# Performance work log

Measured on AMD Instinct MI355X. Metric: run time of the kernel, lower is better.

## Reference

```python
import jax, jax.numpy as jnp
import numpy as np
from jax import lax

B, T, D, H, HODE = 1024, 128, 64, 256, 256
DT = 0.1  # times spaced by 0.1 == integration_step_size -> one RK4 step per interval


def setup_inputs() -> dict:
    key = jax.random.key(0)
    ks = jax.random.split(key, 10)
    s = lambda fan: 1.0 / np.sqrt(fan)
    return {
        "x": jax.random.normal(ks[0], (B, T, D), jnp.float32),
        "times": jnp.arange(T, dtype=jnp.float32) * DT,
        "mask": (jax.random.uniform(ks[1], (B, T)) > 0.3).astype(jnp.float32),
        # ODE MLP: Linear(H->HODE), ReLU, Linear(HODE->H)
        "W1": jax.random.uniform(ks[2], (HODE, H), jnp.float32, -s(H), s(H)),
        "b1": jax.random.uniform(ks[3], (HODE,), jnp.float32, -s(H), s(H)),
        "W2": jax.random.uniform(ks[4], (H, HODE), jnp.float32, -s(HODE), s(HODE)),
        "b2": jax.random.uniform(ks[5], (H,), jnp.float32, -s(HODE), s(HODE)),
        # GRUCell params (torch layout: [3H, D]/[3H, H], gate order r,z,n)
        "W_ih": jax.random.uniform(ks[6], (3 * H, D), jnp.float32, -s(H), s(H)),
        "b_ih": jax.random.uniform(ks[7], (3 * H,), jnp.float32, -s(H), s(H)),
        "W_hh": jax.random.uniform(ks[8], (3 * H, H), jnp.float32, -s(H), s(H)),
        "b_hh": jax.random.uniform(ks[9], (3 * H,), jnp.float32, -s(H), s(H)),
    }


def _ode_gru_forward(x, times, mask, W1, b1, W2, b2, W_ih, b_ih, W_hh, b_hh):
    Bs, Ts, _ = x.shape
    Hs = W_hh.shape[1]

    def f(h):  # autonomous ODE vector field: MLP(h)
        return jnp.maximum(h @ W1.T + b1, 0.0) @ W2.T + b2

    def rk4_step(h, dt):
        k1 = f(h)
        k2 = f(h + 0.5 * dt * k1)
        k3 = f(h + 0.5 * dt * k2)
        k4 = f(h + dt * k3)
        return h + (dt / 6.0) * (k1 + 2.0 * k2 + 2.0 * k3 + k4)

    def gru_update(xt, h, m):
        gi = xt @ W_ih.T + b_ih  # [B, 3H]
        gh = h @ W_hh.T + b_hh
        i_r, i_z, i_n = jnp.split(gi, 3, axis=-1)
        h_r, h_z, h_n = jnp.split(gh, 3, axis=-1)
        r = jax.nn.sigmoid(i_r + h_r)
        z = jax.nn.sigmoid(i_z + h_z)
        n = jnp.tanh(i_n + r * h_n)
        h_next = (1.0 - z) * n + z * h
        m = m[:, None]
        return m * h_next + (1.0 - m) * h

    h0 = gru_update(x[:, 0], jnp.zeros((Bs, Hs), x.dtype), mask[:, 0])
    dts = times[1:] - times[:-1]  # [T-1]

    def step(h, inp):
        xt, mt, dt = inp
        h_ode = rk4_step(h, dt)
        h = gru_update(xt, h_ode, mt)
        return h, h

    xs = (jnp.swapaxes(x[:, 1:], 0, 1), jnp.swapaxes(mask[:, 1:], 0, 1), dts)
    _, hs = lax.scan(step, h0, xs)  # hs: [T-1, B, H]
    out = jnp.concatenate([h0[None], hs], axis=0)  # [T, B, H]
    return jnp.swapaxes(out, 0, 1)  # [B, T, H]


def reference(x, times, mask, W1, b1, W2, b2, W_ih, b_ih, W_hh, b_hh):
    return _ode_gru_forward(x, times, mask, W1, b1, W2, b2, W_ih, b_ih, W_hh, b_hh)
```

## Files before the change

kernel.cpp:

```cpp
#include <hip/hip_runtime.h>
#include <math.h>

#define TT_ 128
#define DD 64
#define HH 256
#define BB 16
#define NBLK 64
#define NTHR 512

#define SA 260
#define SX 68
#define SG 516

typedef short bf16x8 __attribute__((ext_vector_type(8)));
typedef float f32x4 __attribute__((ext_vector_type(4)));
typedef unsigned int uint;
typedef unsigned short ushort;
typedef uint u32x4 __attribute__((ext_vector_type(4)));

__device__ ushort g_W1p[16 * 8 * 2 * 512];
__device__ ushort g_W2p[16 * 8 * 2 * 512];
__device__ ushort g_Wrzp[32 * 10 * 2 * 512];
__device__ ushort g_Whnp[16 * 8 * 2 * 512];
__device__ ushort g_Winp[16 * 2 * 512];

__device__ __forceinline__ ushort bf16_rne(float f) {
  uint u = __builtin_bit_cast(uint, f);
  return (ushort)((u + 0x7fffu + ((u >> 16) & 1u)) >> 16);
}
__device__ __forceinline__ float bf16_f32(ushort h) {
  uint u = ((uint)h) << 16;
  return __builtin_bit_cast(float, u);
}

__global__ __launch_bounds__(256) void prep(
    const float* __restrict__ W1, const float* __restrict__ W2,
    const float* __restrict__ Wih, const float* __restrict__ Whh)
{
  const int s = blockIdx.x * 256 + threadIdx.x;
  const int S1 = 16 * 8 * 512;
  const int S2 = S1 + 16 * 8 * 512;
  const int S3 = S2 + 32 * 10 * 512;
  const int S4 = S3 + 16 * 8 * 512;
  const int S5 = S4 + 16 * 2 * 512;
  if (s >= S5) return;

  if (s < S2) {
    const int r = (s < S1) ? s : s - S1;
    const int t = r / (8 * 512);
    const int o = (r / 512) & 7;
    const int pos = r & 511;
    const int l = pos >> 3, j = pos & 7;
    const int n = t * 16 + (l & 15);
    const int k = o * 32 + (l >> 4) * 8 + j;
    const float w = (s < S1) ? W1[n * HH + k] : W2[n * HH + k];
    ushort hi = bf16_rne(w);
    ushort lo = bf16_rne(w - bf16_f32(hi));
    ushort* dst = (s < S1) ? g_W1p : g_W2p;
    dst[((t * 8 + o) * 2) * 512 + pos] = hi;
    dst[((t * 8 + o) * 2 + 1) * 512 + pos] = lo;
  } else if (s < S3) {
    const int r = s - S2;
    const int t = r / (10 * 512);
    const int o = (r / 512) % 10;
    const int pos = r & 511;
    const int l = pos >> 3, j = pos & 7;
    const int n = t * 16 + (l & 15);
    float w;
    if (o < 8) w = Whh[n * HH + o * 32 + (l >> 4) * 8 + j];
    else       w = Wih[n * DD + (o - 8) * 32 + (l >> 4) * 8 + j];
    ushort hi = bf16_rne(w);
    ushort lo = bf16_rne(w - bf16_f32(hi));
    g_Wrzp[((t * 10 + o) * 2) * 512 + pos] = hi;
    g_Wrzp[((t * 10 + o) * 2 + 1) * 512 + pos] = lo;
  } else if (s < S4) {
    const int r = s - S3;
    const int t = r / (8 * 512);
    const int o = (r / 512) & 7;
    const int pos = r & 511;
    const int l = pos >> 3, j = pos & 7;
    const int n = 512 + t * 16 + (l & 15);
    const float w = Whh[n * HH + o * 32 + (l >> 4) * 8 + j];
    ushort hi = bf16_rne(w);
    ushort lo = bf16_rne(w - bf16_f32(hi));
    g_Whnp[((t * 8 + o) * 2) * 512 + pos] = hi;
    g_Whnp[((t * 8 + o) * 2 + 1) * 512 + pos] = lo;
  } else {
    const int r = s - S4;
    const int t = r / (2 * 512);
    const int o = (r / 512) & 1;
    const int pos = r & 511;
    const int l = pos >> 3, j = pos & 7;
    const int n = 512 + t * 16 + (l & 15);
    const float w = Wih[n * DD + o * 32 + (l >> 4) * 8 + j];
    g_Winp[(t * 2 + o) * 512 + pos] = bf16_rne(w);
  }
}

__device__ __forceinline__ void build_frags(const float* __restrict__ ap,
                                            bf16x8& ahi, bf16x8& alo)
{
  const float4 a0 = *(const float4*)ap;
  const float4 a1 = *(const float4*)(ap + 4);
  float af[8] = {a0.x, a0.y, a0.z, a0.w, a1.x, a1.y, a1.z, a1.w};
  uint hu[4], lu[4];
#pragma unroll
  for (int jj = 0; jj < 4; ++jj) {
    const uint ue = __builtin_bit_cast(uint, af[2 * jj]);
    const uint uo = __builtin_bit_cast(uint, af[2 * jj + 1]);
    hu[jj] = (ue >> 16) | (uo & 0xffff0000u);
    const float he = __builtin_bit_cast(float, ue & 0xffff0000u);
    const float ho = __builtin_bit_cast(float, uo & 0xffff0000u);
    const uint le = __builtin_bit_cast(uint, af[2 * jj] - he);
    const uint lo = __builtin_bit_cast(uint, af[2 * jj + 1] - ho);
    lu[jj] = (le >> 16) | (lo & 0xffff0000u);
  }
  u32x4 hv = {hu[0], hu[1], hu[2], hu[3]};
  u32x4 lv = {lu[0], lu[1], lu[2], lu[3]};
  ahi = __builtin_bit_cast(bf16x8, hv);
  alo = __builtin_bit_cast(bf16x8, lv);
}

#define MFMA(A, B, C) __builtin_amdgcn_mfma_f32_16x16x32_bf16((A), (B), (C), 0, 0, 0)

__device__ __forceinline__ void mm2t3(const float* __restrict__ src, int stride,
                                      const ushort* __restrict__ pack, int t0,
                                      int lane, f32x4& acc0, f32x4& acc1)
{
  const int l15 = lane & 15, lq = lane >> 4;
  const ushort* pb = pack + lane * 8;
#pragma unroll
  for (int o = 0; o < 8; ++o) {
    bf16x8 ahi, alo;
    build_frags(src + l15 * stride + o * 32 + lq * 8, ahi, alo);
    const ushort* p0 = pb + ((t0 * 8 + o) * 2) * 512;
    const ushort* p1 = pb + (((t0 + 1) * 8 + o) * 2) * 512;
    const bf16x8 w0h = *(const bf16x8*)p0;
    const bf16x8 w0l = *(const bf16x8*)(p0 + 512);
    const bf16x8 w1h = *(const bf16x8*)p1;
    const bf16x8 w1l = *(const bf16x8*)(p1 + 512);
    acc0 = MFMA(ahi, w0h, acc0);
    acc1 = MFMA(ahi, w1h, acc1);
    acc0 = MFMA(alo, w0h, acc0);
    acc1 = MFMA(alo, w1h, acc1);
    acc0 = MFMA(ahi, w0l, acc0);
    acc1 = MFMA(ahi, w1l, acc1);
  }
}

__device__ __forceinline__ void mm_rz(const float* __restrict__ hsrc,
                                      const float* __restrict__ xsrc,
                                      int lane, int w, f32x4 az[4])
{
  const int l15 = lane & 15, lq = lane >> 4;
  const ushort* pb = g_Wrzp + lane * 8;
#pragma unroll
  for (int o = 0; o < 8; ++o) {
    bf16x8 ahi, alo;
    build_frags(hsrc + l15 * SA + o * 32 + lq * 8, ahi, alo);
#pragma unroll
    for (int q = 0; q < 4; ++q) {
      const int t = 4 * w + q;
      const ushort* p = pb + ((t * 10 + o) * 2) * 512;
      const bf16x8 wh = *(const bf16x8*)p;
      const bf16x8 wl = *(const bf16x8*)(p + 512);
      az[q] = MFMA(ahi, wh, az[q]);
      az[q] = MFMA(alo, wh, az[q]);
      az[q] = MFMA(ahi, wl, az[q]);
    }
  }
#pragma unroll
  for (int o = 0; o < 2; ++o) {
    bf16x8 ahi, alo;
    build_frags(xsrc + l15 * SX + o * 32 + lq * 8, ahi, alo);
#pragma unroll
    for (int q = 0; q < 4; ++q) {
      const int t = 4 * w + q;
      const ushort* p = pb + ((t * 10 + 8 + o) * 2) * 512;
      const bf16x8 wh = *(const bf16x8*)p;
      az[q] = MFMA(ahi, wh, az[q]);
      az[q] = MFMA(alo, wh, az[q]);
    }
  }
}

__device__ __forceinline__ void mm_in_f(const float* __restrict__ xsrc,
                                        int lane, int t0, f32x4& acc0, f32x4& acc1)
{
  const int l15 = lane & 15, lq = lane >> 4;
#pragma unroll
  for (int o = 0; o < 2; ++o) {
    bf16x8 ahi, alo;
    build_frags(xsrc + l15 * SX + o * 32 + lq * 8, ahi, alo);
    const bf16x8 w0 = *(const bf16x8*)(g_Winp + (t0 * 2 + o) * 512 + lane * 8);
    const bf16x8 w1 = *(const bf16x8*)(g_Winp + ((t0 + 1) * 2 + o) * 512 + lane * 8);
    acc0 = MFMA(ahi, w0, acc0);
    acc0 = MFMA(alo, w0, acc0);
    acc1 = MFMA(ahi, w1, acc1);
    acc1 = MFMA(alo, w1, acc1);
  }
}

__global__ __launch_bounds__(NTHR, 2) void odegru_kernel(
    const float* __restrict__ x, const float* __restrict__ times,
    const float* __restrict__ mask,
    const float* __restrict__ b1, const float* __restrict__ b2,
    const float* __restrict__ bih, const float* __restrict__ bhh,
    float* __restrict__ out)
{
  __shared__ __align__(16) float sAh[BB * SA];
  __shared__ __align__(16) float sAin[BB * SA];
  __shared__ __align__(16) float sU[BB * SA];
  __shared__ __align__(16) float sX[BB * SX];
  __shared__ __align__(16) float sGRZ[BB * SG];
  __shared__ __align__(16) float sGHN[BB * SA];
  __shared__ __align__(16) float sGIN[BB * SA];

  const int tid = threadIdx.x;
  const int lane = tid & 63;
  const int w = tid >> 6;
  const int l15 = lane & 15;
  const int lq = lane >> 4;
  const int b0 = blockIdx.x * BB;

  const int c0 = (2 * w) * 16 + l15;
  const int c1 = (2 * w + 1) * 16 + l15;
  const float b1c0 = b1[c0], b1c1 = b1[c1];
  const float b2c0 = b2[c0], b2c1 = b2[c1];

  const int pi = tid & 255;
  const int pb0 = (tid >> 8) * 8;
  const float brz_r = bih[pi] + bhh[pi];
  const float brz_z = bih[pi + 256] + bhh[pi + 256];
  const float bn_i = bih[pi + 512];
  const float bn_h = bhh[pi + 512];

  const f32x4 Z = {0.f, 0.f, 0.f, 0.f};

  auto feval = [&](const float* src, f32x4& kv0, f32x4& kv1) {
    f32x4 a0 = Z, a1 = Z;
    mm2t3(src, SA, g_W1p, 2 * w, lane, a0, a1);
#pragma unroll
    for (int r = 0; r < 4; ++r) {
      const int b = lq * 4 + r;
      sU[b * SA + c0] = fmaxf(a0[r] + b1c0, 0.f);
      sU[b * SA + c1] = fmaxf(a1[r] + b1c1, 0.f);
    }
    __syncthreads();
    f32x4 p0 = Z, p1 = Z;
    mm2t3(sU, SA, g_W2p, 2 * w, lane, p0, p1);
    kv0 = p0 + b2c0;
    kv1 = p1 + b2c1;
  };

  auto wAin = [&](float coef, const f32x4& v0, const f32x4& v1) {
#pragma unroll
    for (int r = 0; r < 4; ++r) {
      const int b = lq * 4 + r;
      sAin[b * SA + c0] = sAh[b * SA + c0] + coef * v0[r];
      sAin[b * SA + c1] = sAh[b * SA + c1] + coef * v1[r];
    }
  };

  for (int t = 0; t < TT_; ++t) {
    {
      const int b = tid >> 5, d = (tid & 31) * 2;
      const float2 v = *(const float2*)&x[((size_t)(b0 + b) * TT_ + t) * DD + d];
      sX[b * SX + d] = v.x;
      sX[b * SX + d + 1] = v.y;
    }
    if (t == 0) {
#pragma unroll
      for (int q = 0; q < 8; ++q) {
        const int idx = tid * 8 + q;
        sAin[(idx >> 8) * SA + (idx & 255)] = 0.f;
      }
    }
    __syncthreads();

    if (t > 0) {
      const float dtv = times[t] - times[t - 1];
      f32x4 kv0, kv1, ks0, ks1;
      feval(sAh, kv0, kv1);
      ks0 = kv0; ks1 = kv1;
      wAin(0.5f * dtv, kv0, kv1);
      __syncthreads();
      feval(sAin, kv0, kv1);
      ks0 += 2.0f * kv0; ks1 += 2.0f * kv1;
      wAin(0.5f * dtv, kv0, kv1);
      __syncthreads();
      feval(sAin, kv0, kv1);
      ks0 += 2.0f * kv0; ks1 += 2.0f * kv1;
      wAin(dtv, kv0, kv1);
      __syncthreads();
      feval(sAin, kv0, kv1);
      ks0 += kv0; ks1 += kv1;
      wAin(dtv * (1.0f / 6.0f), ks0, ks1);
      __syncthreads();
    }

    {
      f32x4 az[4] = {Z, Z, Z, Z};
      mm_rz(sAin, sX, lane, w, az);
#pragma unroll
      for (int q = 0; q < 4; ++q)
#pragma unroll
        for (int r = 0; r < 4; ++r) {
          const int b = lq * 4 + r;
          sGRZ[b * SG + (4 * w + q) * 16 + l15] = az[q][r];
        }
      f32x4 h0 = Z, h1 = Z;
      mm2t3(sAin, SA, g_Whnp, 2 * w, lane, h0, h1);
      f32x4 i0 = Z, i1 = Z;
      mm_in_f(sX, lane, 2 * w, i0, i1);
#pragma unroll
      for (int r = 0; r < 4; ++r) {
        const int b = lq * 4 + r;
        sGHN[b * SA + c0] = h0[r];
        sGHN[b * SA + c1] = h1[r];
        sGIN[b * SA + c0] = i0[r];
        sGIN[b * SA + c1] = i1[r];
      }
    }
    __syncthreads();

#pragma unroll
    for (int bb = 0; bb < 8; ++bb) {
      const int b = pb0 + bb;
      const float gr = sGRZ[b * SG + pi] + brz_r;
      const float gz = sGRZ[b * SG + pi + 256] + brz_z;
      const float hn = sGHN[b * SA + pi] + bn_h;
      const float gn = sGIN[b * SA + pi] + bn_i;
      const float hode = sAin[b * SA + pi];
      const float rg = 1.f / (1.f + __expf(-gr));
      const float zg = 1.f / (1.f + __expf(-gz));
      const float ng = 1.f - 2.f / (__expf(2.f * (gn + rg * hn)) + 1.f);
      const float hnext = (1.f - zg) * ng + zg * hode;
      const float m = mask[(size_t)(b0 + b) * TT_ + t];
      const float hnew = m * hnext + (1.f - m) * hode;
      sAh[b * SA + pi] = hnew;
      out[((size_t)(b0 + b) * TT_ + t) * HH + pi] = hnew;
    }
    __syncthreads();
  }
}

extern "C" void kernel_launch(void* const* d_in, const int* in_sizes, int n_in,
                              void* d_out, int out_size, void* d_ws, size_t ws_size,
                              hipStream_t stream) {
  (void)in_sizes; (void)n_in; (void)d_ws; (void)ws_size; (void)out_size;
  const float* x     = (const float*)d_in[0];
  const float* times = (const float*)d_in[1];
  const float* mask  = (const float*)d_in[2];
  const float* W1    = (const float*)d_in[3];
  const float* b1    = (const float*)d_in[4];
  const float* W2    = (const float*)d_in[5];
  const float* b2    = (const float*)d_in[6];
  const float* Wih   = (const float*)d_in[7];
  const float* bih   = (const float*)d_in[8];
  const float* Whh   = (const float*)d_in[9];
  const float* bhh   = (const float*)d_in[10];
  float* out = (float*)d_out;

  hipLaunchKernelGGL(prep, dim3((376832 + 255) / 256), dim3(256), 0, stream,
                     W1, W2, Wih, Whh);
  hipLaunchKernelGGL(odegru_kernel, dim3(NBLK), dim3(NTHR), 0, stream,
                     x, times, mask, b1, b2, bih, bhh, out);
}
```

Before: 7.528 ms.

## Store bf16 hi/lo split activations in LDS and fuse GRU gates into MFMA epilogue

Activations are now split into bf16 hi/lo once, when they are written to shared memory, so each matmul no longer re-splits fp32 values while building its fragments. The block grows to 1024 threads with one 16-column tile per wave. Because each wave then owns all r/z/n gates for its columns, the GRU nonlinearity runs directly on the MFMA accumulators and the gate staging buffers in shared memory go away. Barriers are replaced by a lighter waitcnt+s_barrier macro and the mask is preloaded into shared memory, at the cost of higher register pressure and a single block per CU at 1024 threads.

Result: faster. 6.858 ms (-8.9%).

```diff
diff --git a/kernel.cpp b/kernel.cpp
--- a/kernel.cpp
+++ b/kernel.cpp
@@ -6,17 +6,16 @@
 #define HH 256
 #define BB 16
 #define NBLK 64
-#define NTHR 512
+#define NTHR 1024
 
 #define SA 260
-#define SX 68
-#define SG 516
+#define SB 264
+#define SXB 72
 
 typedef short bf16x8 __attribute__((ext_vector_type(8)));
 typedef float f32x4 __attribute__((ext_vector_type(4)));
 typedef unsigned int uint;
 typedef unsigned short ushort;
-typedef uint u32x4 __attribute__((ext_vector_type(4)));
 
 __device__ ushort g_W1p[16 * 8 * 2 * 512];
 __device__ ushort g_W2p[16 * 8 * 2 * 512];
@@ -31,6 +30,12 @@
 __device__ __forceinline__ float bf16_f32(ushort h) {
   uint u = ((uint)h) << 16;
   return __builtin_bit_cast(float, u);
+}
+__device__ __forceinline__ void hl_split(float f, ushort& hi, ushort& lo) {
+  const uint u = __builtin_bit_cast(uint, f);
+  hi = (ushort)(u >> 16);
+  const float fh = __builtin_bit_cast(float, u & 0xffff0000u);
+  lo = (ushort)(__builtin_bit_cast(uint, f - fh) >> 16);
 }
 
 __global__ __launch_bounds__(256) void prep(
@@ -97,111 +102,81 @@
   }
 }
 
-__device__ __forceinline__ void build_frags(const float* __restrict__ ap,
-                                            bf16x8& ahi, bf16x8& alo)
-{
-  const float4 a0 = *(const float4*)ap;
-  const float4 a1 = *(const float4*)(ap + 4);
-  float af[8] = {a0.x, a0.y, a0.z, a0.w, a1.x, a1.y, a1.z, a1.w};
-  uint hu[4], lu[4];
-#pragma unroll
-  for (int jj = 0; jj < 4; ++jj) {
-    const uint ue = __builtin_bit_cast(uint, af[2 * jj]);
-    const uint uo = __builtin_bit_cast(uint, af[2 * jj + 1]);
-    hu[jj] = (ue >> 16) | (uo & 0xffff0000u);
-    const float he = __builtin_bit_cast(float, ue & 0xffff0000u);
-    const float ho = __builtin_bit_cast(float, uo & 0xffff0000u);
-    const uint le = __builtin_bit_cast(uint, af[2 * jj] - he);
-    const uint lo = __builtin_bit_cast(uint, af[2 * jj + 1] - ho);
-    lu[jj] = (le >> 16) | (lo & 0xffff0000u);
-  }
-  u32x4 hv = {hu[0], hu[1], hu[2], hu[3]};
-  u32x4 lv = {lu[0], lu[1], lu[2], lu[3]};
-  ahi = __builtin_bit_cast(bf16x8, hv);
-  alo = __builtin_bit_cast(bf16x8, lv);
-}
-
 #define MFMA(A, B, C) __builtin_amdgcn_mfma_f32_16x16x32_bf16((A), (B), (C), 0, 0, 0)
 
-__device__ __forceinline__ void mm2t3(const float* __restrict__ src, int stride,
-                                      const ushort* __restrict__ pack, int t0,
-                                      int lane, f32x4& acc0, f32x4& acc1)
-{
-  const int l15 = lane & 15, lq = lane >> 4;
-  const ushort* pb = pack + lane * 8;
+#define LBAR() asm volatile("s_waitcnt lgkmcnt(0)\ns_barrier" ::: "memory")
+
+__device__ __forceinline__ f32x4 mm1(const ushort* __restrict__ Ahi,
+                                     const ushort* __restrict__ Alo,
+                                     const ushort* __restrict__ pack,
+                                     int tile, int lane, f32x4 acc)
+{
+  const int aoff = (lane & 15) * SB + (lane >> 4) * 8;
+  const ushort* wp = pack + (size_t)tile * 8192 + lane * 8;
 #pragma unroll
   for (int o = 0; o < 8; ++o) {
-    bf16x8 ahi, alo;
-    build_frags(src + l15 * stride + o * 32 + lq * 8, ahi, alo);
-    const ushort* p0 = pb + ((t0 * 8 + o) * 2) * 512;
-    const ushort* p1 = pb + (((t0 + 1) * 8 + o) * 2) * 512;
-    const bf16x8 w0h = *(const bf16x8*)p0;
-    const bf16x8 w0l = *(const bf16x8*)(p0 + 512);
-    const bf16x8 w1h = *(const bf16x8*)p1;
-    const bf16x8 w1l = *(const bf16x8*)(p1 + 512);
-    acc0 = MFMA(ahi, w0h, acc0);
-    acc1 = MFMA(ahi, w1h, acc1);
-    acc0 = MFMA(alo, w0h, acc0);
-    acc1 = MFMA(alo, w1h, acc1);
-    acc0 = MFMA(ahi, w0l, acc0);
-    acc1 = MFMA(ahi, w1l, acc1);
-  }
-}
-
-__device__ __forceinline__ void mm_rz(const float* __restrict__ hsrc,
-                                      const float* __restrict__ xsrc,
-                                      int lane, int w, f32x4 az[4])
-{
-  const int l15 = lane & 15, lq = lane >> 4;
-  const ushort* pb = g_Wrzp + lane * 8;
+    const bf16x8 ah = *(const bf16x8*)(Ahi + aoff + o * 32);
+    const bf16x8 al = *(const bf16x8*)(Alo + aoff + o * 32);
+    const bf16x8 wh = *(const bf16x8*)(wp + o * 1024);
+    const bf16x8 wl = *(const bf16x8*)(wp + o * 1024 + 512);
+    acc = MFMA(ah, wh, acc);
+    acc = MFMA(al, wh, acc);
+    acc = MFMA(ah, wl, acc);
+  }
+  return acc;
+}
+
+__device__ __forceinline__ void mm_rz(const ushort* __restrict__ Ahi,
+                                      const ushort* __restrict__ Alo,
+                                      const ushort* __restrict__ Xhi,
+                                      const ushort* __restrict__ Xlo,
+                                      int wv, int lane, f32x4& ar, f32x4& az)
+{
+  const int aoff = (lane & 15) * SB + (lane >> 4) * 8;
+  const int xoff = (lane & 15) * SXB + (lane >> 4) * 8;
+  const ushort* pr = g_Wrzp + (size_t)wv * 10240 + lane * 8;
+  const ushort* pz = g_Wrzp + (size_t)(16 + wv) * 10240 + lane * 8;
 #pragma unroll
   for (int o = 0; o < 8; ++o) {
-    bf16x8 ahi, alo;
-    build_frags(hsrc + l15 * SA + o * 32 + lq * 8, ahi, alo);
-#pragma unroll
-    for (int q = 0; q < 4; ++q) {
-      const int t = 4 * w + q;
-      const ushort* p = pb + ((t * 10 + o) * 2) * 512;
-      const bf16x8 wh = *(const bf16x8*)p;
-      const bf16x8 wl = *(const bf16x8*)(p + 512);
-      az[q] = MFMA(ahi, wh, az[q]);
-      az[q] = MFMA(alo, wh, az[q]);
-      az[q] = MFMA(ahi, wl, az[q]);
-    }
+    const bf16x8 ah = *(const bf16x8*)(Ahi + aoff + o * 32);
+    const bf16x8 al = *(const bf16x8*)(Alo + aoff + o * 32);
+    const bf16x8 wrh = *(const bf16x8*)(pr + o * 1024);
+    const bf16x8 wrl = *(const bf16x8*)(pr + o * 1024 + 512);
+    const bf16x8 wzh = *(const bf16x8*)(pz + o * 1024);
+    const bf16x8 wzl = *(const bf16x8*)(pz + o * 1024 + 512);
+    ar = MFMA(ah, wrh, ar); az = MFMA(ah, wzh, az);
+    ar = MFMA(al, wrh, ar); az = MFMA(al, wzh, az);
+    ar = MFMA(ah, wrl, ar); az = MFMA(ah, wzl, az);
   }
 #pragma unroll
   for (int o = 0; o < 2; ++o) {
-    bf16x8 ahi, alo;
-    build_frags(xsrc + l15 * SX + o * 32 + lq * 8, ahi, alo);
-#pragma unroll
-    for (int q = 0; q < 4; ++q) {
-      const int t = 4 * w + q;
-      const ushort* p = pb + ((t * 10 + 8 + o) * 2) * 512;
-      const bf16x8 wh = *(const bf16x8*)p;
-      az[q] = MFMA(ahi, wh, az[q]);
-      az[q] = MFMA(alo, wh, az[q]);
-    }
-  }
-}
-
-__device__ __forceinline__ void mm_in_f(const float* __restrict__ xsrc,
-                                        int lane, int t0, f32x4& acc0, f32x4& acc1)
-{
-  const int l15 = lane & 15, lq = lane >> 4;
+    const bf16x8 xh = *(const bf16x8*)(Xhi + xoff + o * 32);
+    const bf16x8 xl = *(const bf16x8*)(Xlo + xoff + o * 32);
+    const bf16x8 wrh = *(const bf16x8*)(pr + (8 + o) * 1024);
+    const bf16x8 wzh = *(const bf16x8*)(pz + (8 + o) * 1024);
+    ar = MFMA(xh, wrh, ar); az = MFMA(xh, wzh, az);
+    ar = MFMA(xl, wrh, ar); az = MFMA(xl, wzh, az);
+  }
+}
+
+__device__ __forceinline__ f32x4 mm_in(const ushort* __restrict__ Xhi,
+                                       const ushort* __restrict__ Xlo,
+                                       int wv, int lane, f32x4 acc)
+{
+  const int xoff = (lane & 15) * SXB + (lane >> 4) * 8;
+  const ushort* pw = g_Winp + (size_t)wv * 1024 + lane * 8;
 #pragma unroll
   for (int o = 0; o < 2; ++o) {
-    bf16x8 ahi, alo;
-    build_frags(xsrc + l15 * SX + o * 32 + lq * 8, ahi, alo);
-    const bf16x8 w0 = *(const bf16x8*)(g_Winp + (t0 * 2 + o) * 512 + lane * 8);
-    const bf16x8 w1 = *(const bf16x8*)(g_Winp + ((t0 + 1) * 2 + o) * 512 + lane * 8);
-    acc0 = MFMA(ahi, w0, acc0);
-    acc0 = MFMA(alo, w0, acc0);
-    acc1 = MFMA(ahi, w1, acc1);
-    acc1 = MFMA(alo, w1, acc1);
-  }
-}
-
-__global__ __launch_bounds__(NTHR, 2) void odegru_kernel(
+    const bf16x8 xh = *(const bf16x8*)(Xhi + xoff + o * 32);
+    const bf16x8 xl = *(const bf16x8*)(Xlo + xoff + o * 32);
+    const bf16x8 w = *(const bf16x8*)(pw + o * 512);
+    acc = MFMA(xh, w, acc);
+    acc = MFMA(xl, w, acc);
+  }
+  return acc;
+}
+
+__global__ __launch_bounds__(NTHR) void odegru_kernel(
     const float* __restrict__ x, const float* __restrict__ times,
     const float* __restrict__ mask,
     const float* __restrict__ b1, const float* __restrict__ b2,
@@ -210,138 +185,128 @@
 {
   __shared__ __align__(16) float sAh[BB * SA];
   __shared__ __align__(16) float sAin[BB * SA];
-  __shared__ __align__(16) float sU[BB * SA];
-  __shared__ __align__(16) float sX[BB * SX];
-  __shared__ __align__(16) float sGRZ[BB * SG];
-  __shared__ __align__(16) float sGHN[BB * SA];
-  __shared__ __align__(16) float sGIN[BB * SA];
+  __shared__ __align__(16) ushort sAhh[BB * SB], sAhl[BB * SB];
+  __shared__ __align__(16) ushort sAinh[BB * SB], sAinl[BB * SB];
+  __shared__ __align__(16) ushort sUh[BB * SB], sUl[BB * SB];
+  __shared__ __align__(16) ushort sXh[BB * SXB], sXl[BB * SXB];
+  __shared__ __align__(16) float sM[BB * TT_];
 
   const int tid = threadIdx.x;
   const int lane = tid & 63;
-  const int w = tid >> 6;
+  const int wv = tid >> 6;
   const int l15 = lane & 15;
   const int lq = lane >> 4;
   const int b0 = blockIdx.x * BB;
 
-  const int c0 = (2 * w) * 16 + l15;
-  const int c1 = (2 * w + 1) * 16 + l15;
-  const float b1c0 = b1[c0], b1c1 = b1[c1];
-  const float b2c0 = b2[c0], b2c1 = b2[c1];
-
-  const int pi = tid & 255;
-  const int pb0 = (tid >> 8) * 8;
-  const float brz_r = bih[pi] + bhh[pi];
-  const float brz_z = bih[pi + 256] + bhh[pi + 256];
-  const float bn_i = bih[pi + 512];
-  const float bn_h = bhh[pi + 512];
+  const int c = wv * 16 + l15;
+  const float b1c = b1[c];
+  const float b2c = b2[c];
+  const float brz_r = bih[c] + bhh[c];
+  const float brz_z = bih[c + 256] + bhh[c + 256];
+  const float bn_i = bih[c + 512];
+  const float bn_h = bhh[c + 512];
 
   const f32x4 Z = {0.f, 0.f, 0.f, 0.f};
 
-  auto feval = [&](const float* src, f32x4& kv0, f32x4& kv1) {
-    f32x4 a0 = Z, a1 = Z;
-    mm2t3(src, SA, g_W1p, 2 * w, lane, a0, a1);
-#pragma unroll
-    for (int r = 0; r < 4; ++r) {
-      const int b = lq * 4 + r;
-      sU[b * SA + c0] = fmaxf(a0[r] + b1c0, 0.f);
-      sU[b * SA + c1] = fmaxf(a1[r] + b1c1, 0.f);
-    }
-    __syncthreads();
-    f32x4 p0 = Z, p1 = Z;
-    mm2t3(sU, SA, g_W2p, 2 * w, lane, p0, p1);
-    kv0 = p0 + b2c0;
-    kv1 = p1 + b2c1;
+  sM[tid] = mask[(size_t)b0 * TT_ + tid];
+  sM[tid + 1024] = mask[(size_t)b0 * TT_ + tid + 1024];
+
+  auto feval = [&](const ushort* Ahi, const ushort* Alo, f32x4& kv) {
+    f32x4 a = mm1(Ahi, Alo, g_W1p, wv, lane, Z);
+#pragma unroll
+    for (int q = 0; q < 4; ++q) {
+      const int b = lq * 4 + q;
+      const float u = fmaxf(a[q] + b1c, 0.f);
+      ushort hi, lo; hl_split(u, hi, lo);
+      sUh[b * SB + c] = hi;
+      sUl[b * SB + c] = lo;
+    }
+    LBAR();
+    f32x4 p = mm1(sUh, sUl, g_W2p, wv, lane, Z);
+    kv = p + b2c;
   };
 
-  auto wAin = [&](float coef, const f32x4& v0, const f32x4& v1) {
-#pragma unroll
-    for (int r = 0; r < 4; ++r) {
-      const int b = lq * 4 + r;
-      sAin[b * SA + c0] = sAh[b * SA + c0] + coef * v0[r];
-      sAin[b * SA + c1] = sAh[b * SA + c1] + coef * v1[r];
+  auto wAin = [&](float coef, const f32x4& v) {
+#pragma unroll
+    for (int q = 0; q < 4; ++q) {
+      const int b = lq * 4 + q;
+      const float nv = sAh[b * SA + c] + coef * v[q];
+      sAin[b * SA + c] = nv;
+      ushort hi, lo; hl_split(nv, hi, lo);
+      sAinh[b * SB + c] = hi;
+      sAinl[b * SB + c] = lo;
     }
   };
 
   for (int t = 0; t < TT_; ++t) {
     {
-      const int b = tid >> 5, d = (tid & 31) * 2;
-      const float2 v = *(const float2*)&x[((size_t)(b0 + b) * TT_ + t) * DD + d];
-      sX[b * SX + d] = v.x;
-      sX[b * SX + d + 1] = v.y;
+      const int b = tid >> 6, d = tid & 63;
+      const float v = x[((size_t)(b0 + b) * TT_ + t) * DD + d];
+      ushort hi, lo; hl_split(v, hi, lo);
+      sXh[b * SXB + d] = hi;
+      sXl[b * SXB + d] = lo;
     }
     if (t == 0) {
-#pragma unroll
-      for (int q = 0; q < 8; ++q) {
-        const int idx = tid * 8 + q;
-        sAin[(idx >> 8) * SA + (idx & 255)] = 0.f;
+      const int cc = tid & 255;
+#pragma unroll
+      for (int q = 0; q < 4; ++q) {
+        const int b = (tid >> 8) * 4 + q;
+        sAin[b * SA + cc] = 0.f;
+        sAinh[b * SB + cc] = 0;
+        sAinl[b * SB + cc] = 0;
       }
     }
-    __syncthreads();
+    LBAR();
 
     if (t > 0) {
       const float dtv = times[t] - times[t - 1];
-      f32x4 kv0, kv1, ks0, ks1;
-      feval(sAh, kv0, kv1);
-      ks0 = kv0; ks1 = kv1;
-      wAin(0.5f * dtv, kv0, kv1);
-      __syncthreads();
-      feval(sAin, kv0, kv1);
-      ks0 += 2.0f * kv0; ks1 += 2.0f * kv1;
-      wAin(0.5f * dtv, kv0, kv1);
-      __syncthreads();
-      feval(sAin, kv0, kv1);
-      ks0 += 2.0f * kv0; ks1 += 2.0f * kv1;
-      wAin(dtv, kv0, kv1);
-      __syncthreads();
-      feval(sAin, kv0, kv1);
-      ks0 += kv0; ks1 += kv1;
-      wAin(dtv * (1.0f / 6.0f), ks0, ks1);
-      __syncthreads();
+      f32x4 kv, ks;
+      feval(sAhh, sAhl, kv);
+      ks = kv;
+      wAin(0.5f * dtv, kv);
+      LBAR();
+      feval(sAinh, sAinl, kv);
+      ks += 2.0f * kv;
+      wAin(0.5f * dtv, kv);
+      LBAR();
+      feval(sAinh, sAinl, kv);
+      ks += 2.0f * kv;
+      wAin(dtv, kv);
+      LBAR();
+      feval(sAinh, sAinl, kv);
+      ks += kv;
+      wAin(dtv * (1.0f / 6.0f), ks);
+      LBAR();
     }
 
     {
-      f32x4 az[4] = {Z, Z, Z, Z};
-      mm_rz(sAin, sX, lane, w, az);
-#pragma unroll
-      for (int q = 0; q < 4; ++q)
-#pragma unroll
-        for (int r = 0; r < 4; ++r) {
-          const int b = lq * 4 + r;
-          sGRZ[b * SG + (4 * w + q) * 16 + l15] = az[q][r];
-        }
-      f32x4 h0 = Z, h1 = Z;
-      mm2t3(sAin, SA, g_Whnp, 2 * w, lane, h0, h1);
-      f32x4 i0 = Z, i1 = Z;
-      mm_in_f(sX, lane, 2 * w, i0, i1);
-#pragma unroll
-      for (int r = 0; r < 4; ++r) {
-        const int b = lq * 4 + r;
-        sGHN[b * SA + c0] = h0[r];
-        sGHN[b * SA + c1] = h1[r];
-        sGIN[b * SA + c0] = i0[r];
-        sGIN[b * SA + c1] = i1[r];
+      f32x4 ar = Z, az = Z;
+      mm_rz(sAinh, sAinl, sXh, sXl, wv, lane, ar, az);
+      f32x4 ahn = mm1(sAinh, sAinl, g_Whnp, wv, lane, Z);
+      f32x4 ain = mm_in(sXh, sXl, wv, lane, Z);
+
+#pragma unroll
+      for (int q = 0; q < 4; ++q) {
+        const int b = lq * 4 + q;
+        const float gr = ar[q] + brz_r;
+        const float gz = az[q] + brz_z;
+        const float hn = ahn[q] + bn_h;
+        const float gn = ain[q] + bn_i;
+        const float hode = sAin[b * SA + c];
+        const float rg = 1.f / (1.f + __expf(-gr));
+        const float zg = 1.f / (1.f + __expf(-gz));
+        const float ng = 1.f - 2.f / (__expf(2.f * (gn + rg * hn)) + 1.f);
+        const float hnext = (1.f - zg) * ng + zg * hode;
+        const float m = sM[b * TT_ + t];
+        const float hnew = m * hnext + (1.f - m) * hode;
+        out[((size_t)(b0 + b) * TT_ + t) * HH + c] = hnew;
+        sAh[b * SA + c] = hnew;
+        ushort hi, lo; hl_split(hnew, hi, lo);
+        sAhh[b * SB + c] = hi;
+        sAhl[b * SB + c] = lo;
       }
     }
-    __syncthreads();
-
-#pragma unroll
-    for (int bb = 0; bb < 8; ++bb) {
-      const int b = pb0 + bb;
-      const float gr = sGRZ[b * SG + pi] + brz_r;
-      const float gz = sGRZ[b * SG + pi + 256] + brz_z;
-      const float hn = sGHN[b * SA + pi] + bn_h;
-      const float gn = sGIN[b * SA + pi] + bn_i;
-      const float hode = sAin[b * SA + pi];
-      const float rg = 1.f / (1.f + __expf(-gr));
-      const float zg = 1.f / (1.f + __expf(-gz));
-      const float ng = 1.f - 2.f / (__expf(2.f * (gn + rg * hn)) + 1.f);
-      const float hnext = (1.f - zg) * ng + zg * hode;
-      const float m = mask[(size_t)(b0 + b) * TT_ + t];
-      const float hnew = m * hnext + (1.f - m) * hode;
-      sAh[b * SA + pi] = hnew;
-      out[((size_t)(b0 + b) * TT_ + t) * HH + pi] = hnew;
-    }
-    __syncthreads();
+    LBAR();
   }
 }
 
```
